# Optimization experiments

Measured on AMD Instinct MI355X. Metric: run time of the kernel, lower is better.

Reference implementation:

```python
import jax, jax.numpy as jnp
import numpy as np

B, S, IN_DIM, OUT_DIM = 16, 1024, 1024, 1024
NEG_SLOPE = 0.01  # torch F.leaky_relu default


def setup_inputs() -> dict:
    key = jax.random.key(0)
    ks = jax.random.split(key, 10)
    sc_in = 1.0 / np.sqrt(IN_DIM)
    sc_out = 1.0 / np.sqrt(OUT_DIM)
    return {
        "xs": jax.random.normal(ks[0], (B, S, IN_DIM), dtype=jnp.float32),
        "mask": jax.random.randint(ks[1], (B, S), 0, 2, dtype=jnp.int32),
        "Wk": jax.random.uniform(ks[2], (OUT_DIM, IN_DIM), jnp.float32, -sc_in, sc_in),
        "bk": jax.random.uniform(ks[3], (OUT_DIM,), jnp.float32, -sc_in, sc_in),
        "Wq": jax.random.uniform(ks[4], (OUT_DIM, IN_DIM), jnp.float32, -sc_in, sc_in),
        "bq": jax.random.uniform(ks[5], (OUT_DIM,), jnp.float32, -sc_in, sc_in),
        "Wv": jax.random.uniform(ks[6], (OUT_DIM, IN_DIM), jnp.float32, -sc_in, sc_in),
        "bv": jax.random.uniform(ks[7], (OUT_DIM,), jnp.float32, -sc_in, sc_in),
        "Wlin": jax.random.uniform(ks[8], (OUT_DIM, OUT_DIM), jnp.float32, -sc_out, sc_out),
        "blin": jax.random.uniform(ks[9], (OUT_DIM,), jnp.float32, -sc_out, sc_out),
    }


def reference(xs, mask, Wk, bk, Wq, bq, Wv, bv, Wlin, blin):
    # projections: torch Linear is x @ W.T + b
    K = jnp.einsum('bsi,oi->bso', xs, Wk) + bk  # [B,S,D]
    Q = jnp.einsum('bsi,oi->bso', xs, Wq) + bq  # [B,S,D]
    V = jnp.einsum('bsi,oi->bso', xs, Wv) + bv  # [B,S,D]
    # qk[b,s,e] = sum_d K[b,s,d] * Q[b,e,d]
    qk = jnp.einsum('bsd,bed->bse', K, Q) / xs.shape[-1]
    # mask.repeat(1,S).view(B,S,S) => element [b,i,j] = mask[b,j] (column/key mask)
    qk = jnp.where(mask[:, None, :].astype(bool), qk, -jnp.inf)
    a = jax.nn.softmax(qk, axis=-1)  # [B,S,S]
    # faithful to einsum('bij,bik->bik'): sum a over last axis, scale V elementwise
    attn = jnp.sum(a, axis=-1, keepdims=True) * V  # [B,S,D]
    out = jnp.einsum('bsd,od->bso', attn, Wlin) + blin
    return jnp.where(out >= 0, out, NEG_SLOPE * out)
```

## Files before the change

kernel.cpp:

```cpp
#include <hip/hip_runtime.h>
#include <hip/hip_bf16.h>
#include <stdint.h>


#define M_TOT 16384
#define KDIM  1024
#define NDIM  1024
#define NKT   32

typedef __attribute__((ext_vector_type(8))) short bf16x8;
typedef __attribute__((ext_vector_type(4))) float f32x4;
typedef __attribute__((ext_vector_type(4))) unsigned short u16x4;
typedef __attribute__((ext_vector_type(8))) unsigned short u16x8;

static __device__ __forceinline__ unsigned short f2bf(float f) {
    union { float f; unsigned int u; } v; v.f = f;
    unsigned int u = v.u;
    return (unsigned short)((u + 0x7fffu + ((u >> 16) & 1u)) >> 16);
}

static __device__ __forceinline__ u16x8 pack8(float4 a, float4 b) {
    u16x8 p = { f2bf(a.x), f2bf(a.y), f2bf(a.z), f2bf(a.w),
                f2bf(b.x), f2bf(b.y), f2bf(b.z), f2bf(b.w) };
    return p;
}

static __device__ __forceinline__ void gload16(const void* g, void* l) {
    __builtin_amdgcn_global_load_lds(
        (__attribute__((address_space(1))) void*)(g),
        (__attribute__((address_space(3))) void*)(l), 16, 0, 0);
}

static __device__ __forceinline__ int swz(int p) {
    return p ^ (((p >> 9) & 1) << 5) ^ (((p >> 8) & 1) << 4);
}

__global__ __launch_bounds__(256) void prep0_kernel(
    const float* __restrict__ Wv, const float* __restrict__ Wlin,
    const float* __restrict__ bv, const float* __restrict__ blin,
    unsigned short* __restrict__ Wvt, unsigned short* __restrict__ Wlb,
    float* __restrict__ bcomb) {
    __shared__ float Tl[64 * 65];
    const int bid = blockIdx.x;
    const int t = threadIdx.x;

    if (bid < 256) {
        const int dt = bid >> 4;
        const int it = bid & 15;
        const int r = t >> 2;
        const int c0 = (t & 3) * 16;
        #pragma unroll
        for (int u = 0; u < 4; ++u) {
            float4 v = *(const float4*)&Wv[((size_t)(dt * 64 + r)) * NDIM + it * 64 + c0 + 4 * u];
            Tl[r * 65 + c0 + 4 * u + 0] = v.x;
            Tl[r * 65 + c0 + 4 * u + 1] = v.y;
            Tl[r * 65 + c0 + 4 * u + 2] = v.z;
            Tl[r * 65 + c0 + 4 * u + 3] = v.w;
        }
        __syncthreads();
        const int i = t >> 2;
        const int dq = (t & 3) * 16;
        float v[16];
        #pragma unroll
        for (int u = 0; u < 16; ++u) v[u] = Tl[(dq + u) * 65 + i];
        u16x8 p0 = { f2bf(v[0]), f2bf(v[1]), f2bf(v[2]), f2bf(v[3]),
                     f2bf(v[4]), f2bf(v[5]), f2bf(v[6]), f2bf(v[7]) };
        u16x8 p1 = { f2bf(v[8]), f2bf(v[9]), f2bf(v[10]), f2bf(v[11]),
                     f2bf(v[12]), f2bf(v[13]), f2bf(v[14]), f2bf(v[15]) };
        unsigned short* dst = &Wvt[((size_t)(it * 64 + i)) * KDIM + dt * 64 + dq];
        *(u16x8*)dst = p0;
        *(u16x8*)(dst + 8) = p1;
    } else if (bid < 512) {
        const size_t idx = (((size_t)(bid - 256)) * 256 + t) * 16;
        float4 a = *(const float4*)&Wlin[idx];
        float4 b = *(const float4*)&Wlin[idx + 4];
        float4 c = *(const float4*)&Wlin[idx + 8];
        float4 d = *(const float4*)&Wlin[idx + 12];
        *(u16x8*)&Wlb[idx] = pack8(a, b);
        *(u16x8*)&Wlb[idx + 8] = pack8(c, d);
    } else {
        const int wave = t >> 6, lane = t & 63;
        const int o = (bid - 512) * 4 + wave;
        float s = 0.f;
        for (int d = lane; d < KDIM; d += 64) s += Wlin[o * KDIM + d] * bv[d];
        #pragma unroll
        for (int off = 32; off > 0; off >>= 1) s += __shfl_down(s, off, 64);
        if (lane == 0) bcomb[o] = s + blin[o];
    }
}

__global__ __launch_bounds__(256) void wcomb_kernel(
    const unsigned short* __restrict__ Wlb, const unsigned short* __restrict__ Wvt,
    unsigned short* __restrict__ Wc) {
    __shared__ unsigned short As[64 * 32];
    __shared__ unsigned short Bs[64 * 32];
    const int t = threadIdx.x;
    const int ot = blockIdx.x >> 4;
    const int it = blockIdx.x & 15;
    const int w = t >> 6, l = t & 63;
    const int wr = (w >> 1) * 32, wc = (w & 1) * 32;
    const int lr = l & 15, lk = l >> 4;

    f32x4 acc[2][2] = {};

    const unsigned short* gA = &Wlb[((size_t)(ot * 64 + (t >> 2))) * KDIM + (t & 3) * 8];
    const unsigned short* gB = &Wvt[((size_t)(it * 64 + (t >> 2))) * KDIM + (t & 3) * 8];
    unsigned short* lA = &As[w * 512];
    unsigned short* lB = &Bs[w * 512];

    for (int kt = 0; kt < KDIM / 32; ++kt) {
        gload16(gA + kt * 32, lA);
        gload16(gB + kt * 32, lB);
        __syncthreads();
        bf16x8 af[2], bfr[2];
        #pragma unroll
        for (int fi = 0; fi < 2; ++fi)
            af[fi] = *(bf16x8*)&As[(wr + fi * 16 + lr) * 32 + lk * 8];
        #pragma unroll
        for (int fj = 0; fj < 2; ++fj)
            bfr[fj] = *(bf16x8*)&Bs[(wc + fj * 16 + lr) * 32 + lk * 8];
        #pragma unroll
        for (int fi = 0; fi < 2; ++fi)
            #pragma unroll
            for (int fj = 0; fj < 2; ++fj)
                acc[fi][fj] = __builtin_amdgcn_mfma_f32_16x16x32_bf16(
                    af[fi], bfr[fj], acc[fi][fj], 0, 0, 0);
        __syncthreads();
    }
    #pragma unroll
    for (int fi = 0; fi < 2; ++fi)
        #pragma unroll
        for (int fj = 0; fj < 2; ++fj)
            #pragma unroll
            for (int r = 0; r < 4; ++r) {
                const int o = ot * 64 + wr + fi * 16 + lk * 4 + r;
                const int i = it * 64 + wc + fj * 16 + lr;
                Wc[(size_t)o * KDIM + i] = f2bf(acc[fi][fj][r]);
            }
}

__global__ __launch_bounds__(512, 2) void main_fused(
    const float* __restrict__ xs, const unsigned short* __restrict__ Wc,
    const float* __restrict__ bcomb, float* __restrict__ out) {
    extern __shared__ char lds[];
    const int tid = threadIdx.x;
    const int w = tid >> 6, l = tid & 63;
    const int wm = w >> 2, wn = w & 3;
    const int lr = l & 15, lk = l >> 4;

    const int swzb = ((blockIdx.x & 7) << 5) + (blockIdx.x >> 3);
    const int mt = swzb >> 2, nt = swzb & 3;

    int aoff[8], boff[4];
    #pragma unroll
    for (int fi = 0; fi < 8; ++fi)
        aoff[fi] = swz((wm * 128 + fi * 16 + lr) * 64 + lk * 16);
    #pragma unroll
    for (int fj = 0; fj < 4; ++fj)
        boff[fj] = 16384 + swz((wn * 64 + fj * 16 + lr) * 64 + lk * 16);

    const float* gAq[2];
    const char* gBq[2];
    #pragma unroll
    for (int c = 0; c < 2; ++c) {
        const int q = c * 8192 + tid * 16;
        const int p = swz(q);
        const int row = p >> 6;
        const int colb = p & 63;
        gAq[c] = xs + ((size_t)(mt * 256 + row)) * KDIM + (colb >> 1);
        gBq[c] = (const char*)Wc + ((size_t)(nt * 256 + row)) * 2048 + colb;
    }
    const int ldsA0 = tid * 16;
    const int ldsA1 = 8192 + tid * 16;
    const int ldsBw = 16384 + w * 1024;

    f32x4 acc[8][4] = {};
    float4 avA[4];

#define LOAD_A(TT)                                                             \
    do {                                                                       \
        avA[0] = *(const float4*)(gAq[0] + (TT) * 32);                         \
        avA[1] = *(const float4*)(gAq[0] + (TT) * 32 + 4);                     \
        avA[2] = *(const float4*)(gAq[1] + (TT) * 32);                         \
        avA[3] = *(const float4*)(gAq[1] + (TT) * 32 + 4);                     \
    } while (0)

#define CVT_A(BUF)                                                             \
    do {                                                                       \
        *(u16x8*)((BUF) + ldsA0) = pack8(avA[0], avA[1]);                      \
        *(u16x8*)((BUF) + ldsA1) = pack8(avA[2], avA[3]);                      \
    } while (0)

#define GLOAD_B(TT, BUF)                                                       \
    do {                                                                       \
        gload16(gBq[0] + (size_t)(TT) * 64, (BUF) + ldsBw);                    \
        gload16(gBq[1] + (size_t)(TT) * 64, (BUF) + 8192 + ldsBw);             \
    } while (0)

    LOAD_A(0);
    GLOAD_B(0, lds);
    CVT_A(lds);
    LOAD_A(1);
    GLOAD_B(1, lds + 32768);
    CVT_A(lds + 32768);
    asm volatile("s_waitcnt lgkmcnt(0)" ::: "memory");
    __builtin_amdgcn_s_barrier();

#define MFMA16(ACCI, AF, BF)                                                   \
    _Pragma("unroll")                                                          \
    for (int fi = 0; fi < 4; ++fi)                                             \
        _Pragma("unroll")                                                      \
        for (int fj = 0; fj < 4; ++fj)                                         \
            acc[(ACCI) + fi][fj] = __builtin_amdgcn_mfma_f32_16x16x32_bf16(    \
                (AF)[fi], (BF)[fj], acc[(ACCI) + fi][fj], 0, 0, 0)

#define ITER(T, SEN, WN)                                                       \
    do {                                                                       \
        const char* cbuf = lds + (size_t)((T) & 3) * 32768;                    \
        char* stbuf = lds + (size_t)(((T) + 2) & 3) * 32768;                   \
                  \
        if (SEN) { LOAD_A((T) + 2); }                                          \
        bf16x8 bfr[4], afr[4];                                                 \
        _Pragma("unroll")                                                      \
        for (int fj = 0; fj < 4; ++fj)                                         \
            bfr[fj] = *(const bf16x8*)(cbuf + boff[fj]);                       \
        _Pragma("unroll")                                                      \
        for (int fi = 0; fi < 4; ++fi)                                         \
            afr[fi] = *(const bf16x8*)(cbuf + aoff[fi]);                       \
        __builtin_amdgcn_s_barrier();                                          \
        __builtin_amdgcn_s_setprio(1);                                         \
        MFMA16(0, afr, bfr);                                                   \
        __builtin_amdgcn_s_setprio(0);                                         \
        __builtin_amdgcn_s_barrier();                                          \
                          \
        if (SEN) { GLOAD_B((T) + 2, stbuf); }                                  \
        bf16x8 af2[4];                                                         \
        _Pragma("unroll")                                                      \
        for (int fi = 0; fi < 4; ++fi)                                         \
            af2[fi] = *(const bf16x8*)(cbuf + aoff[4 + fi]);                   \
        __builtin_amdgcn_s_barrier();                                          \
        __builtin_amdgcn_s_setprio(1);                                         \
        MFMA16(4, af2, bfr);                                                   \
        __builtin_amdgcn_s_setprio(0);                                         \
            \
        if (SEN) { CVT_A(stbuf); }                                             \
                                                            \
        asm volatile("s_waitcnt vmcnt(" #WN ")" ::: "memory");                 \
        asm volatile("s_waitcnt lgkmcnt(0)" ::: "memory");                     \
        __builtin_amdgcn_s_barrier();                                          \
    } while (0)

    for (int t = 0; t < NKT - 2; ++t) {
        ITER(t, 1, 2);
    }
    ITER(30, 0, 2);
    ITER(31, 0, 0);
#undef ITER
#undef MFMA16
#undef GLOAD_B
#undef CVT_A
#undef LOAD_A

    #pragma unroll
    for (int fi = 0; fi < 8; ++fi)
        #pragma unroll
        for (int fj = 0; fj < 4; ++fj) {
            const int col = nt * 256 + wn * 64 + fj * 16 + lr;
            const float b = bcomb[col];
            #pragma unroll
            for (int r = 0; r < 4; ++r) {
                const int row = mt * 256 + wm * 128 + fi * 16 + lk * 4 + r;
                float v = acc[fi][fj][r] + b;
                out[(size_t)row * NDIM + col] = v >= 0.f ? v : 0.01f * v;
            }
        }
}

__global__ __launch_bounds__(256) void main_gemm_f32(
    const float* __restrict__ X, const unsigned short* __restrict__ Wc,
    const float* __restrict__ bcomb, float* __restrict__ out) {
    __shared__ unsigned short As[128 * 32];
    __shared__ unsigned short Bs[128 * 32];
    const int t = threadIdx.x;
    const int nt = blockIdx.x & 7;
    const int mt = blockIdx.x >> 3;
    const int w = t >> 6, l = t & 63;
    const int wr = (w >> 1) * 64, wcc = (w & 1) * 64;
    const int lr = l & 15, lk = l >> 4;

    f32x4 acc[4][4] = {};

    const int arow = t >> 3;
    const int akq = t & 7;
    const int brow = t >> 2;
    const int bc4 = t & 3;

    for (int kt = 0; kt < KDIM / 32; ++kt) {
        float4 av[4];
        #pragma unroll
        for (int j = 0; j < 4; ++j) {
            const int row = j * 32 + arow;
            av[j] = *(const float4*)&X[(mt * 128 + row) * KDIM + kt * 32 + akq * 4];
        }
        __syncthreads();
        #pragma unroll
        for (int j = 0; j < 4; ++j) {
            const int row = j * 32 + arow;
            u16x4 p = { f2bf(av[j].x), f2bf(av[j].y), f2bf(av[j].z), f2bf(av[j].w) };
            *(u16x4*)&As[row * 32 + akq * 4] = p;
        }
        #pragma unroll
        for (int j = 0; j < 2; ++j) {
            const int row = j * 64 + brow;
            const unsigned short* g = &Wc[(nt * 128 + row) * KDIM + kt * 32 + bc4 * 8];
            unsigned short* ldst = &Bs[(j * 256 + w * 64) * 8];
            gload16(g, ldst);
        }
        __syncthreads();
        bf16x8 af[4], bfr[4];
        #pragma unroll
        for (int fi = 0; fi < 4; ++fi)
            af[fi] = *(bf16x8*)&As[(wr + fi * 16 + lr) * 32 + lk * 8];
        #pragma unroll
        for (int fj = 0; fj < 4; ++fj)
            bfr[fj] = *(bf16x8*)&Bs[(wcc + fj * 16 + lr) * 32 + lk * 8];
        #pragma unroll
        for (int fi = 0; fi < 4; ++fi)
            #pragma unroll
            for (int fj = 0; fj < 4; ++fj)
                acc[fi][fj] = __builtin_amdgcn_mfma_f32_16x16x32_bf16(
                    af[fi], bfr[fj], acc[fi][fj], 0, 0, 0);
    }

    #pragma unroll
    for (int fi = 0; fi < 4; ++fi)
        #pragma unroll
        for (int fj = 0; fj < 4; ++fj) {
            const int col = nt * 128 + wcc + fj * 16 + lr;
            const float b = bcomb[col];
            #pragma unroll
            for (int r = 0; r < 4; ++r) {
                const int row = mt * 128 + wr + fi * 16 + lk * 4 + r;
                float v = acc[fi][fj][r] + b;
                out[row * NDIM + col] = v >= 0.f ? v : 0.01f * v;
            }
        }
}

extern "C" void kernel_launch(void* const* d_in, const int* in_sizes, int n_in,
                              void* d_out, int out_size, void* d_ws, size_t ws_size,
                              hipStream_t stream) {
    const float* xs   = (const float*)d_in[0];
    const float* Wv   = (const float*)d_in[6];
    const float* bv   = (const float*)d_in[7];
    const float* Wlin = (const float*)d_in[8];
    const float* blin = (const float*)d_in[9];

    unsigned short* Wc = (unsigned short*)d_ws;
    float* bcomb = (float*)((char*)d_ws + 2097152);
    float* out = (float*)d_out;

    unsigned short* Wvt = (unsigned short*)d_out;
    unsigned short* Wlb = (unsigned short*)((char*)d_out + 2097152);

    const size_t NEED = 2101248;
    hipLaunchKernelGGL(prep0_kernel, dim3(768), dim3(256), 0, stream,
                       Wv, Wlin, bv, blin, Wvt, Wlb, bcomb);
    hipLaunchKernelGGL(wcomb_kernel, dim3(256), dim3(256), 0, stream,
                       Wlb, Wvt, Wc);
    if (ws_size >= NEED) {
        (void)hipFuncSetAttribute((const void*)main_fused,
                                  hipFuncAttributeMaxDynamicSharedMemorySize,
                                  131072);
        hipLaunchKernelGGL(main_fused, dim3(256), dim3(512), 131072, stream,
                           xs, Wc, bcomb, out);
    } else {
        hipLaunchKernelGGL(main_gemm_f32, dim3((M_TOT / 128) * (NDIM / 128)),
                           dim3(256), 0, stream, xs, Wc, bcomb, out);
    }
}
```

Before: 82.21 us.

## Replace pipelined 256x256 fused GEMM with simple single-buffered 128x128 tile kernel

The main fused GEMM drops its 4-stage LDS ring buffer, split-phase MFMA scheduling, priority hints and 256x256 tiles with 512 threads. It becomes a straightforward 128x128-tile kernel with 256 threads, 16 KB of static LDS, and two __syncthreads per K-step. The aim is higher occupancy and simpler scheduling. In exchange it loses the overlap of global loads with MFMA work and gets less data reuse per tile.

```diff
diff --git a/kernel.cpp b/kernel.cpp
--- a/kernel.cpp
+++ b/kernel.cpp
@@ -6,7 +6,6 @@
 #define M_TOT 16384
 #define KDIM  1024
 #define NDIM  1024
-#define NKT   32
 
 typedef __attribute__((ext_vector_type(8))) short bf16x8;
 typedef __attribute__((ext_vector_type(4))) float f32x4;
@@ -139,137 +138,80 @@
             }
 }
 
-__global__ __launch_bounds__(512, 2) void main_fused(
+__global__ __launch_bounds__(256) void main_fused(
     const float* __restrict__ xs, const unsigned short* __restrict__ Wc,
     const float* __restrict__ bcomb, float* __restrict__ out) {
-    extern __shared__ char lds[];
-    const int tid = threadIdx.x;
-    const int w = tid >> 6, l = tid & 63;
-    const int wm = w >> 2, wn = w & 3;
+    __shared__ __align__(16) char As[8192];
+    __shared__ __align__(16) char Bs[8192];
+    const int t = threadIdx.x;
+    const int w = t >> 6, l = t & 63;
+    const int wm = w >> 1, wn = w & 1;
     const int lr = l & 15, lk = l >> 4;
 
-    const int swzb = ((blockIdx.x & 7) << 5) + (blockIdx.x >> 3);
-    const int mt = swzb >> 2, nt = swzb & 3;
-
-    int aoff[8], boff[4];
-    #pragma unroll
-    for (int fi = 0; fi < 8; ++fi)
-        aoff[fi] = swz((wm * 128 + fi * 16 + lr) * 64 + lk * 16);
+    const int swzb = ((blockIdx.x & 7) << 7) + (blockIdx.x >> 3);
+    const int mt = swzb >> 3, nt = swzb & 7;
+
+    int aoff[4], boff[4];
+    #pragma unroll
+    for (int fi = 0; fi < 4; ++fi)
+        aoff[fi] = swz((wm * 64 + fi * 16 + lr) * 64 + lk * 16);
     #pragma unroll
     for (int fj = 0; fj < 4; ++fj)
-        boff[fj] = 16384 + swz((wn * 64 + fj * 16 + lr) * 64 + lk * 16);
+        boff[fj] = swz((wn * 64 + fj * 16 + lr) * 64 + lk * 16);
 
     const float* gAq[2];
+    #pragma unroll
+    for (int c = 0; c < 2; ++c) {
+        const int q = c * 4096 + t * 16;
+        const int p = swz(q);
+        gAq[c] = xs + ((size_t)(mt * 128 + (p >> 6))) * KDIM + ((p & 63) >> 1);
+    }
     const char* gBq[2];
     #pragma unroll
     for (int c = 0; c < 2; ++c) {
-        const int q = c * 8192 + tid * 16;
+        const int q = c * 4096 + w * 1024 + l * 16;
         const int p = swz(q);
-        const int row = p >> 6;
-        const int colb = p & 63;
-        gAq[c] = xs + ((size_t)(mt * 256 + row)) * KDIM + (colb >> 1);
-        gBq[c] = (const char*)Wc + ((size_t)(nt * 256 + row)) * 2048 + colb;
-    }
-    const int ldsA0 = tid * 16;
-    const int ldsA1 = 8192 + tid * 16;
-    const int ldsBw = 16384 + w * 1024;
-
-    f32x4 acc[8][4] = {};
-    float4 avA[4];
-
-#define LOAD_A(TT)                                                             \
-    do {                                                                       \
-        avA[0] = *(const float4*)(gAq[0] + (TT) * 32);                         \
-        avA[1] = *(const float4*)(gAq[0] + (TT) * 32 + 4);                     \
-        avA[2] = *(const float4*)(gAq[1] + (TT) * 32);                         \
-        avA[3] = *(const float4*)(gAq[1] + (TT) * 32 + 4);                     \
-    } while (0)
-
-#define CVT_A(BUF)                                                             \
-    do {                                                                       \
-        *(u16x8*)((BUF) + ldsA0) = pack8(avA[0], avA[1]);                      \
-        *(u16x8*)((BUF) + ldsA1) = pack8(avA[2], avA[3]);                      \
-    } while (0)
-
-#define GLOAD_B(TT, BUF)                                                       \
-    do {                                                                       \
-        gload16(gBq[0] + (size_t)(TT) * 64, (BUF) + ldsBw);                    \
-        gload16(gBq[1] + (size_t)(TT) * 64, (BUF) + 8192 + ldsBw);             \
-    } while (0)
-
-    LOAD_A(0);
-    GLOAD_B(0, lds);
-    CVT_A(lds);
-    LOAD_A(1);
-    GLOAD_B(1, lds + 32768);
-    CVT_A(lds + 32768);
-    asm volatile("s_waitcnt lgkmcnt(0)" ::: "memory");
-    __builtin_amdgcn_s_barrier();
-
-#define MFMA16(ACCI, AF, BF)                                                   \
-    _Pragma("unroll")                                                          \
-    for (int fi = 0; fi < 4; ++fi)                                             \
-        _Pragma("unroll")                                                      \
-        for (int fj = 0; fj < 4; ++fj)                                         \
-            acc[(ACCI) + fi][fj] = __builtin_amdgcn_mfma_f32_16x16x32_bf16(    \
-                (AF)[fi], (BF)[fj], acc[(ACCI) + fi][fj], 0, 0, 0)
-
-#define ITER(T, SEN, WN)                                                       \
-    do {                                                                       \
-        const char* cbuf = lds + (size_t)((T) & 3) * 32768;                    \
-        char* stbuf = lds + (size_t)(((T) + 2) & 3) * 32768;                   \
-                  \
-        if (SEN) { LOAD_A((T) + 2); }                                          \
-        bf16x8 bfr[4], afr[4];                                                 \
-        _Pragma("unroll")                                                      \
-        for (int fj = 0; fj < 4; ++fj)                                         \
-            bfr[fj] = *(const bf16x8*)(cbuf + boff[fj]);                       \
-        _Pragma("unroll")                                                      \
-        for (int fi = 0; fi < 4; ++fi)                                         \
-            afr[fi] = *(const bf16x8*)(cbuf + aoff[fi]);                       \
-        __builtin_amdgcn_s_barrier();                                          \
-        __builtin_amdgcn_s_setprio(1);                                         \
-        MFMA16(0, afr, bfr);                                                   \
-        __builtin_amdgcn_s_setprio(0);                                         \
-        __builtin_amdgcn_s_barrier();                                          \
-                          \
-        if (SEN) { GLOAD_B((T) + 2, stbuf); }                                  \
-        bf16x8 af2[4];                                                         \
-        _Pragma("unroll")                                                      \
-        for (int fi = 0; fi < 4; ++fi)                                         \
-            af2[fi] = *(const bf16x8*)(cbuf + aoff[4 + fi]);                   \
-        __builtin_amdgcn_s_barrier();                                          \
-        __builtin_amdgcn_s_setprio(1);                                         \
-        MFMA16(4, af2, bfr);                                                   \
-        __builtin_amdgcn_s_setprio(0);                                         \
-            \
-        if (SEN) { CVT_A(stbuf); }                                             \
-                                                            \
-        asm volatile("s_waitcnt vmcnt(" #WN ")" ::: "memory");                 \
-        asm volatile("s_waitcnt lgkmcnt(0)" ::: "memory");                     \
-        __builtin_amdgcn_s_barrier();                                          \
-    } while (0)
-
-    for (int t = 0; t < NKT - 2; ++t) {
-        ITER(t, 1, 2);
-    }
-    ITER(30, 0, 2);
-    ITER(31, 0, 0);
-#undef ITER
-#undef MFMA16
-#undef GLOAD_B
-#undef CVT_A
-#undef LOAD_A
-
-    #pragma unroll
-    for (int fi = 0; fi < 8; ++fi)
+        gBq[c] = (const char*)Wc + ((size_t)(nt * 128 + (p >> 6))) * 2048 + (p & 63);
+    }
+
+    f32x4 acc[4][4] = {};
+
+    for (int kt = 0; kt < KDIM / 32; ++kt) {
+        float4 a0 = *(const float4*)(gAq[0] + kt * 32);
+        float4 a1 = *(const float4*)(gAq[0] + kt * 32 + 4);
+        float4 a2 = *(const float4*)(gAq[1] + kt * 32);
+        float4 a3 = *(const float4*)(gAq[1] + kt * 32 + 4);
+        gload16(gBq[0] + (size_t)kt * 64, Bs + w * 1024);
+        gload16(gBq[1] + (size_t)kt * 64, Bs + 4096 + w * 1024);
+        *(u16x8*)(As + t * 16) = pack8(a0, a1);
+        *(u16x8*)(As + 4096 + t * 16) = pack8(a2, a3);
+        __syncthreads();
+
+        bf16x8 af[4], bfr[4];
+        #pragma unroll
+        for (int fi = 0; fi < 4; ++fi)
+            af[fi] = *(const bf16x8*)(As + aoff[fi]);
+        #pragma unroll
+        for (int fj = 0; fj < 4; ++fj)
+            bfr[fj] = *(const bf16x8*)(Bs + boff[fj]);
+        #pragma unroll
+        for (int fi = 0; fi < 4; ++fi)
+            #pragma unroll
+            for (int fj = 0; fj < 4; ++fj)
+                acc[fi][fj] = __builtin_amdgcn_mfma_f32_16x16x32_bf16(
+                    af[fi], bfr[fj], acc[fi][fj], 0, 0, 0);
+        __syncthreads();
+    }
+
+    #pragma unroll
+    for (int fi = 0; fi < 4; ++fi)
         #pragma unroll
         for (int fj = 0; fj < 4; ++fj) {
-            const int col = nt * 256 + wn * 64 + fj * 16 + lr;
+            const int col = nt * 128 + wn * 64 + fj * 16 + lr;
             const float b = bcomb[col];
             #pragma unroll
             for (int r = 0; r < 4; ++r) {
-                const int row = mt * 256 + wm * 128 + fi * 16 + lk * 4 + r;
+                const int row = mt * 128 + wm * 64 + fi * 16 + lk * 4 + r;
                 float v = acc[fi][fj][r] + b;
                 out[(size_t)row * NDIM + col] = v >= 0.f ? v : 0.01f * v;
             }
@@ -369,11 +311,8 @@
     hipLaunchKernelGGL(wcomb_kernel, dim3(256), dim3(256), 0, stream,
                        Wlb, Wvt, Wc);
     if (ws_size >= NEED) {
-        (void)hipFuncSetAttribute((const void*)main_fused,
-                                  hipFuncAttributeMaxDynamicSharedMemorySize,
-                                  131072);
-        hipLaunchKernelGGL(main_fused, dim3(256), dim3(512), 131072, stream,
-                           xs, Wc, bcomb, out);
+        hipLaunchKernelGGL(main_fused, dim3((M_TOT / 128) * (NDIM / 128)),
+                           dim3(256), 0, stream, xs, Wc, bcomb, out);
     } else {
         hipLaunchKernelGGL(main_gemm_f32, dim3((M_TOT / 128) * (NDIM / 128)),
                            dim3(256), 0, stream, xs, Wc, bcomb, out);
```

Result: slower. 98.63 us (+20.0%).

## Prefetch B tiles three stages ahead and switch to 128-byte XOR swizzle

Applied to the files above, without the earlier changes.

The B (weight) tiles, loaded by DMA into LDS, are now prefetched three k-tiles ahead instead of two, while A (fp32 activations converted to bf16) stays two ahead. This uses all four LDS buffers and aims to hide more global-load latency for B. The LDS layout also changes to pack two 64-byte rows into each 128-byte line with an XOR swizzle on bits 7-9, meant to reduce bank conflicts on fragment reads. The prologue and tail iterations are restructured to match, which makes the vmcnt accounting more complex to get right.

```diff
diff --git a/kernel.cpp b/kernel.cpp
--- a/kernel.cpp
+++ b/kernel.cpp
@@ -6,7 +6,7 @@
 #define M_TOT 16384
 #define KDIM  1024
 #define NDIM  1024
-#define NKT   32
+#define NT    32
 
 typedef __attribute__((ext_vector_type(8))) short bf16x8;
 typedef __attribute__((ext_vector_type(4))) float f32x4;
@@ -31,8 +31,8 @@
         (__attribute__((address_space(3))) void*)(l), 16, 0, 0);
 }
 
-static __device__ __forceinline__ int swz(int p) {
-    return p ^ (((p >> 9) & 1) << 5) ^ (((p >> 8) & 1) << 4);
+static __device__ __forceinline__ int swz128(int p) {
+    return p ^ (((p >> 7) & 7) << 4);
 }
 
 __global__ __launch_bounds__(256) void prep0_kernel(
@@ -153,26 +153,37 @@
 
     int aoff[8], boff[4];
     #pragma unroll
-    for (int fi = 0; fi < 8; ++fi)
-        aoff[fi] = swz((wm * 128 + fi * 16 + lr) * 64 + lk * 16);
-    #pragma unroll
-    for (int fj = 0; fj < 4; ++fj)
-        boff[fj] = 16384 + swz((wn * 64 + fj * 16 + lr) * 64 + lk * 16);
+    for (int fi = 0; fi < 8; ++fi) {
+        const int r = wm * 128 + fi * 16 + lr;
+        aoff[fi] = swz128(((r >> 1) << 7) | ((r & 1) << 6) | (lk << 4));
+    }
+    #pragma unroll
+    for (int fj = 0; fj < 4; ++fj) {
+        const int r = wn * 64 + fj * 16 + lr;
+        boff[fj] = 16384 + swz128(((r >> 1) << 7) | ((r & 1) << 6) | (lk << 4));
+    }
 
     const float* gAq[2];
-    const char* gBq[2];
     #pragma unroll
     for (int c = 0; c < 2; ++c) {
         const int q = c * 8192 + tid * 16;
-        const int p = swz(q);
-        const int row = p >> 6;
-        const int colb = p & 63;
-        gAq[c] = xs + ((size_t)(mt * 256 + row)) * KDIM + (colb >> 1);
-        gBq[c] = (const char*)Wc + ((size_t)(nt * 256 + row)) * 2048 + colb;
+        const int p = swz128(q);
+        const int r = ((p >> 7) << 1) | ((p >> 6) & 1);
+        gAq[c] = xs + ((size_t)(mt * 256 + r)) * KDIM + ((p & 63) >> 1);
     }
     const int ldsA0 = tid * 16;
     const int ldsA1 = 8192 + tid * 16;
-    const int ldsBw = 16384 + w * 1024;
+
+    const char* srcB0; const char* srcB1;
+    {
+        const int q0 = 0 * 8192 + w * 1024 + l * 16, p0 = swz128(q0);
+        const int q1 = 1 * 8192 + w * 1024 + l * 16, p1 = swz128(q1);
+        const int r0 = ((p0 >> 7) << 1) | ((p0 >> 6) & 1), c0 = p0 & 63;
+        const int r1 = ((p1 >> 7) << 1) | ((p1 >> 6) & 1), c1 = p1 & 63;
+        srcB0 = (const char*)Wc + ((size_t)(nt * 256 + r0) * KDIM) * 2 + c0;
+        srcB1 = (const char*)Wc + ((size_t)(nt * 256 + r1) * KDIM) * 2 + c1;
+    }
+    const int ldsw = w * 1024;
 
     f32x4 acc[8][4] = {};
     float4 avA[4];
@@ -193,16 +204,18 @@
 
 #define GLOAD_B(TT, BUF)                                                       \
     do {                                                                       \
-        gload16(gBq[0] + (size_t)(TT) * 64, (BUF) + ldsBw);                    \
-        gload16(gBq[1] + (size_t)(TT) * 64, (BUF) + 8192 + ldsBw);             \
+        gload16(srcB0 + (size_t)(TT) * 64, (BUF) + 16384 + ldsw);              \
+        gload16(srcB1 + (size_t)(TT) * 64, (BUF) + 24576 + ldsw);              \
     } while (0)
 
     LOAD_A(0);
-    GLOAD_B(0, lds);
     CVT_A(lds);
     LOAD_A(1);
+    CVT_A(lds + 32768);
+    GLOAD_B(0, lds);
     GLOAD_B(1, lds + 32768);
-    CVT_A(lds + 32768);
+    GLOAD_B(2, lds + 65536);
+    asm volatile("s_waitcnt vmcnt(4)" ::: "memory");
     asm volatile("s_waitcnt lgkmcnt(0)" ::: "memory");
     __builtin_amdgcn_s_barrier();
 
@@ -214,12 +227,13 @@
             acc[(ACCI) + fi][fj] = __builtin_amdgcn_mfma_f32_16x16x32_bf16(    \
                 (AF)[fi], (BF)[fj], acc[(ACCI) + fi][fj], 0, 0, 0)
 
-#define ITER(T, SEN, WN)                                                       \
+#define KTILE(T, SA, SB, WN)                                                   \
     do {                                                                       \
         const char* cbuf = lds + (size_t)((T) & 3) * 32768;                    \
-        char* stbuf = lds + (size_t)(((T) + 2) & 3) * 32768;                   \
-                  \
-        if (SEN) { LOAD_A((T) + 2); }                                          \
+        char* abuf = lds + (size_t)(((T) + 2) & 3) * 32768;                    \
+        char* bbuf = lds + (size_t)(((T) + 3) & 3) * 32768;                    \
+              \
+        if (SA) { LOAD_A((T) + 2); }                                           \
         bf16x8 bfr[4], afr[4];                                                 \
         _Pragma("unroll")                                                      \
         for (int fj = 0; fj < 4; ++fj)                                         \
@@ -233,7 +247,7 @@
         __builtin_amdgcn_s_setprio(0);                                         \
         __builtin_amdgcn_s_barrier();                                          \
                           \
-        if (SEN) { GLOAD_B((T) + 2, stbuf); }                                  \
+        if (SB) { GLOAD_B((T) + 3, bbuf); }                                    \
         bf16x8 af2[4];                                                         \
         _Pragma("unroll")                                                      \
         for (int fi = 0; fi < 4; ++fi)                                         \
@@ -242,20 +256,20 @@
         __builtin_amdgcn_s_setprio(1);                                         \
         MFMA16(4, af2, bfr);                                                   \
         __builtin_amdgcn_s_setprio(0);                                         \
-            \
-        if (SEN) { CVT_A(stbuf); }                                             \
-                                                            \
+                \
+        if (SA) { CVT_A(abuf); }                                               \
         asm volatile("s_waitcnt vmcnt(" #WN ")" ::: "memory");                 \
         asm volatile("s_waitcnt lgkmcnt(0)" ::: "memory");                     \
         __builtin_amdgcn_s_barrier();                                          \
     } while (0)
 
-    for (int t = 0; t < NKT - 2; ++t) {
-        ITER(t, 1, 2);
-    }
-    ITER(30, 0, 2);
-    ITER(31, 0, 0);
-#undef ITER
+    for (int t = 0; t < NT - 3; ++t) {
+        KTILE(t, 1, 1, 2);
+    }
+    KTILE(29, 1, 0, 2);
+    KTILE(30, 0, 0, 0);
+    KTILE(31, 0, 0, 0);
+#undef KTILE
 #undef MFMA16
 #undef GLOAD_B
 #undef CVT_A
```

Result: faster. 78.06 us (-5.0%).
